# Kernel tuning notes

Measured on AMD Instinct MI355X. Metric: run time of the kernel, lower is better.

Reference implementation:

```python
import jax, jax.numpy as jnp
import numpy as np

EPS = 1e-6

def setup_inputs() -> dict:
    key = jax.random.key(0)
    ks = jax.random.split(key, 8)
    B, C, H, W = 8, 256, 128, 128
    d = C // 8  # scale=8
    return {
        "x": jax.random.normal(ks[0], (B, C, H, W), dtype=jnp.float32),
        "wq": jax.random.normal(ks[1], (d, C), dtype=jnp.float32) * 0.05,
        "bq": jax.random.normal(ks[2], (d,), dtype=jnp.float32) * 0.05,
        "wk": jax.random.normal(ks[3], (d, C), dtype=jnp.float32) * 0.05,
        "bk": jax.random.normal(ks[4], (d,), dtype=jnp.float32) * 0.05,
        "wv": jax.random.normal(ks[5], (C, C), dtype=jnp.float32) * 0.05,
        "bv": jax.random.normal(ks[6], (C,), dtype=jnp.float32) * 0.05,
        "gamma": jax.random.normal(ks[7], (1,), dtype=jnp.float32) * 0.05,
    }

def reference(x, wq, bq, wk, bk, wv, bv, gamma):
    B, C, H, W = x.shape
    N = H * W
    xf = x.reshape(B, C, N)  # flatten spatial
    # 1x1 convs == channel-mixing matmuls
    Q = jax.nn.softplus(jnp.einsum('dc,bcn->bnd', wq, xf) + bq[None, None, :])  # [B,N,d]
    K = jax.nn.softplus(jnp.einsum('dc,bcn->bdn', wk, xf) + bk[None, :, None])  # [B,d,N]
    V = jnp.einsum('ec,bcn->ben', wv, xf) + bv[None, :, None]                    # [B,C,N]
    KV = jnp.einsum('bmn,bcn->bmc', K, V)                # [B,d,C]
    norm = 1.0 / jnp.einsum('bnm,bm->bn', Q, K.sum(-1) + EPS)  # [B,N]
    wv_out = jnp.einsum('bnm,bmc,bn->bcn', Q, KV, norm)  # [B,C,N]
    return x + gamma * wv_out.reshape(B, C, H, W)
```

## Files before the change

### kernel.cpp

```cpp
#include <hip/hip_runtime.h>

#define NB 8
#define NC 256
#define ND 32
#define NN 16384
#define EPSF 1e-6f

__device__ __forceinline__ float softplusf(float v) {
    return fmaxf(v, 0.0f) + log1pf(__expf(-fabsf(v)));
}

__global__ __launch_bounds__(256) void kA(
    const float* __restrict__ x, const float* __restrict__ wk,
    const float* __restrict__ bk, float* __restrict__ part,
    float* __restrict__ kxf, float* __restrict__ ksum, int use_part)
{
    __shared__ __align__(16) float xsT[32 * 258];
    __shared__ __align__(16) float wkM[32 * 260];
    __shared__ __align__(16) float Ks [32 * 36];

    const int t    = threadIdx.x;
    const int b    = blockIdx.x >> 6;
    const int tile = blockIdx.x & 63;
    const int n0   = tile << 8;
    const float* xb = x + (size_t)b * NC * NN;

    #pragma unroll
    for (int i = 0; i < 32; ++i) {
        int f = t + (i << 8);
        wkM[(f >> 8) * 260 + (f & 255)] = wk[f];
    }

    const int jA  = t & 31;
    const int m0A = (t >> 5) << 2;
    const int m0X = (t >> 6) << 3;
    const int eX  = t & 63;

    float bkr[4];
    #pragma unroll
    for (int r = 0; r < 4; ++r) bkr[r] = bk[m0A + r];

    float acc[8][4];
    #pragma unroll
    for (int a = 0; a < 8; ++a)
        #pragma unroll
        for (int kk = 0; kk < 4; ++kk) acc[a][kk] = 0.0f;
    float ksacc[4] = {0.f, 0.f, 0.f, 0.f};

    for (int st = 0; st < 8; ++st) {
        const int n1 = n0 + (st << 5);
        __syncthreads();
        #pragma unroll
        for (int i = 0; i < 32; ++i) {
            int f = t + (i << 8);
            int c = f >> 5, j = f & 31;
            xsT[j * 258 + c] = xb[c * NN + n1 + j];
        }
        __syncthreads();

        float kacc[4] = {0.f, 0.f, 0.f, 0.f};
        #pragma unroll 4
        for (int c = 0; c < 256; c += 4) {
            float2 xa = *(const float2*)&xsT[jA * 258 + c];
            float2 xc = *(const float2*)&xsT[jA * 258 + c + 2];
            #pragma unroll
            for (int r = 0; r < 4; ++r) {
                float4 w = *(const float4*)&wkM[(m0A + r) * 260 + c];
                kacc[r] = fmaf(xa.x, w.x, kacc[r]);
                kacc[r] = fmaf(xa.y, w.y, kacc[r]);
                kacc[r] = fmaf(xc.x, w.z, kacc[r]);
                kacc[r] = fmaf(xc.y, w.w, kacc[r]);
            }
        }
        #pragma unroll
        for (int r = 0; r < 4; ++r) {
            float kv_ = softplusf(kacc[r] + bkr[r]);
            Ks[jA * 36 + m0A + r] = kv_;
            ksacc[r] += kv_;
        }
        __syncthreads();

        #pragma unroll 2
        for (int j = 0; j < 32; ++j) {
            const float* kp = &Ks[j * 36 + m0X];
            float4 ka = *(const float4*)kp;
            float4 kb = *(const float4*)(kp + 4);
            const float km[8] = {ka.x, ka.y, ka.z, ka.w, kb.x, kb.y, kb.z, kb.w};
            float xv[4];
            #pragma unroll
            for (int kk = 0; kk < 4; ++kk) xv[kk] = xsT[j * 258 + eX + (kk << 6)];
            #pragma unroll
            for (int a = 0; a < 8; ++a)
                #pragma unroll
                for (int kk = 0; kk < 4; ++kk)
                    acc[a][kk] = fmaf(km[a], xv[kk], acc[a][kk]);
        }
    }

    #pragma unroll
    for (int r = 0; r < 4; ++r) {
        float v = ksacc[r];
        for (int o = 16; o; o >>= 1) v += __shfl_down(v, o, 32);
        if (jA == 0) atomicAdd(&ksum[b * 32 + m0A + r], v);
    }

    if (use_part) {
        float* dst = part + (size_t)blockIdx.x * 8192;
        #pragma unroll
        for (int a = 0; a < 8; ++a)
            #pragma unroll
            for (int kk = 0; kk < 4; ++kk)
                dst[(m0X + a) * 256 + eX + (kk << 6)] = acc[a][kk];
    } else {
        float* dst = kxf + (size_t)b * 8192;
        #pragma unroll
        for (int a = 0; a < 8; ++a)
            #pragma unroll
            for (int kk = 0; kk < 4; ++kk)
                atomicAdd(&dst[(m0X + a) * 256 + eX + (kk << 6)], acc[a][kk]);
    }
}

__global__ __launch_bounds__(256) void kR(const float* __restrict__ part,
                                          float* __restrict__ kxf)
{
    int idx = blockIdx.x * 256 + threadIdx.x;
    int b = idx >> 13, f = idx & 8191;
    float s = 0.f;
    #pragma unroll 8
    for (int tl = 0; tl < 64; ++tl)
        s += part[(size_t)(b * 64 + tl) * 8192 + f];
    kxf[idx] = s;
}

__global__ __launch_bounds__(256) void kB(
    const float* __restrict__ kxf, const float* __restrict__ ksum,
    const float* __restrict__ wv, const float* __restrict__ bv,
    float* __restrict__ kv)
{
    __shared__ float wvT[256 * 33];
    __shared__ float kxs[32 * 257];

    const int t  = threadIdx.x;
    const int b  = blockIdx.x >> 3;
    const int c0 = (blockIdx.x & 7) << 5;

    #pragma unroll
    for (int i = 0; i < 32; ++i) {
        int f = t + (i << 8);
        int r = f >> 8, e = f & 255;
        wvT[e * 33 + r]  = wv[(size_t)(c0 + r) * 256 + e];
        kxs[r * 257 + e] = kxf[b * 8192 + f];
    }
    __syncthreads();

    const int cl = t & 31, mq = t >> 5;
    float a0 = 0.f, a1 = 0.f, a2 = 0.f, a3 = 0.f;
    for (int e = 0; e < 256; ++e) {
        float wvv = wvT[e * 33 + cl];
        a0 = fmaf(kxs[(mq     ) * 257 + e], wvv, a0);
        a1 = fmaf(kxs[(mq +  8) * 257 + e], wvv, a1);
        a2 = fmaf(kxs[(mq + 16) * 257 + e], wvv, a2);
        a3 = fmaf(kxs[(mq + 24) * 257 + e], wvv, a3);
    }
    const int c = c0 + cl;
    const float bvc = bv[c];
    const float* ks = ksum + b * 32;
    float* kvb = kv + (size_t)b * 8192;
    kvb[(mq     ) * 256 + c] = a0 + bvc * ks[mq     ];
    kvb[(mq +  8) * 256 + c] = a1 + bvc * ks[mq +  8];
    kvb[(mq + 16) * 256 + c] = a2 + bvc * ks[mq + 16];
    kvb[(mq + 24) * 256 + c] = a3 + bvc * ks[mq + 24];
}

__global__ __launch_bounds__(512) void kC(
    const float* __restrict__ x, const float* __restrict__ wq,
    const float* __restrict__ bq, const float* __restrict__ kv,
    const float* __restrict__ ksum, const float* __restrict__ gamma,
    float* __restrict__ out)
{
    __shared__ __align__(16) float xs [256 * 64];
    __shared__ __align__(16) float wqM[32 * 260];
    __shared__ __align__(16) float Qs [32 * 68];
    __shared__ __align__(16) float KVs[32 * 256];
    __shared__ float ksE[32];

    const int t    = threadIdx.x;
    const int b    = blockIdx.x >> 6;
    const int tile = blockIdx.x & 63;
    const int n0   = tile << 8;
    const float* xb = x + (size_t)b * NC * NN;
    const float g = gamma[0];

    #pragma unroll
    for (int i = 0; i < 16; ++i) {
        int f = t + (i << 9);
        wqM[(f >> 8) * 260 + (f & 255)] = wq[f];
        KVs[f] = kv[(size_t)b * 8192 + f];
    }
    if (t < 32) ksE[t] = ksum[b * 32 + t] + EPSF;

    const int jsQ = t & 15;
    const int mQ  = t >> 4;
    const float bqm = bq[mQ];
    const int jO  = t & 63;
    const int c0O = (t >> 6) << 5;

    for (int st = 0; st < 4; ++st) {
        const int n1 = n0 + (st << 6);
        __syncthreads();
        #pragma unroll
        for (int i = 0; i < 32; ++i) {
            int f = t + (i << 9);
            int c = f >> 6, j = f & 63;
            xs[f] = xb[c * NN + n1 + j];
        }
        __syncthreads();

        float qa[4] = {0.f, 0.f, 0.f, 0.f};
        #pragma unroll 4
        for (int c = 0; c < 256; c += 4) {
            float4 w  = *(const float4*)&wqM[mQ * 260 + c];
            float4 x0 = *(const float4*)&xs[(c + 0) * 64 + (jsQ << 2)];
            float4 x1 = *(const float4*)&xs[(c + 1) * 64 + (jsQ << 2)];
            float4 x2 = *(const float4*)&xs[(c + 2) * 64 + (jsQ << 2)];
            float4 x3 = *(const float4*)&xs[(c + 3) * 64 + (jsQ << 2)];
            qa[0] = fmaf(w.x, x0.x, qa[0]); qa[0] = fmaf(w.y, x1.x, qa[0]);
            qa[0] = fmaf(w.z, x2.x, qa[0]); qa[0] = fmaf(w.w, x3.x, qa[0]);
            qa[1] = fmaf(w.x, x0.y, qa[1]); qa[1] = fmaf(w.y, x1.y, qa[1]);
            qa[1] = fmaf(w.z, x2.y, qa[1]); qa[1] = fmaf(w.w, x3.y, qa[1]);
            qa[2] = fmaf(w.x, x0.z, qa[2]); qa[2] = fmaf(w.y, x1.z, qa[2]);
            qa[2] = fmaf(w.z, x2.z, qa[2]); qa[2] = fmaf(w.w, x3.z, qa[2]);
            qa[3] = fmaf(w.x, x0.w, qa[3]); qa[3] = fmaf(w.y, x1.w, qa[3]);
            qa[3] = fmaf(w.z, x2.w, qa[3]); qa[3] = fmaf(w.w, x3.w, qa[3]);
        }
        #pragma unroll
        for (int r = 0; r < 4; ++r)
            Qs[mQ * 68 + (jsQ << 2) + r] = softplusf(qa[r] + bqm);
        __syncthreads();

        float q[32];
        #pragma unroll
        for (int m = 0; m < 32; ++m) q[m] = Qs[m * 68 + jO];
        float den = 0.f;
        #pragma unroll
        for (int m = 0; m < 32; ++m) den = fmaf(q[m], ksE[m], den);
        const float nrm = g / den;

        #pragma unroll
        for (int cc = 0; cc < 8; ++cc) {
            const int c = c0O + (cc << 2);
            float s0 = 0.f, s1 = 0.f, s2 = 0.f, s3 = 0.f;
            #pragma unroll
            for (int m = 0; m < 32; ++m) {
                float4 kvv = *(const float4*)&KVs[m * 256 + c];
                s0 = fmaf(q[m], kvv.x, s0);
                s1 = fmaf(q[m], kvv.y, s1);
                s2 = fmaf(q[m], kvv.z, s2);
                s3 = fmaf(q[m], kvv.w, s3);
            }
            size_t base = (size_t)b * NC * NN + (size_t)c * NN + n1 + jO;
            out[base         ] = xs[(c + 0) * 64 + jO] + nrm * s0;
            out[base +     NN] = xs[(c + 1) * 64 + jO] + nrm * s1;
            out[base + 2 * NN] = xs[(c + 2) * 64 + jO] + nrm * s2;
            out[base + 3 * NN] = xs[(c + 3) * 64 + jO] + nrm * s3;
        }
    }
}

extern "C" void kernel_launch(void* const* d_in, const int* in_sizes, int n_in,
                              void* d_out, int out_size, void* d_ws, size_t ws_size,
                              hipStream_t stream)
{
    (void)in_sizes; (void)n_in; (void)out_size;
    const float* x     = (const float*)d_in[0];
    const float* wq    = (const float*)d_in[1];
    const float* bq    = (const float*)d_in[2];
    const float* wk    = (const float*)d_in[3];
    const float* bk    = (const float*)d_in[4];
    const float* wv    = (const float*)d_in[5];
    const float* bv    = (const float*)d_in[6];
    const float* gamma = (const float*)d_in[7];
    float* out = (float*)d_out;

    char* ws = (char*)d_ws;
    float* kxf  = (float*)(ws);
    float* ksum = (float*)(ws + 262144);
    float* kv   = (float*)(ws + 263168);
    float* part = (float*)(ws + 525312);
    const size_t need_part = 525312ull + 512ull * 8192ull * 4ull;
    const int use_part = (ws_size >= need_part) ? 1 : 0;

    hipMemsetAsync(ksum, 0, 1024, stream);
    if (!use_part) hipMemsetAsync(kxf, 0, 262144, stream);

    kA<<<dim3(512), dim3(256), 0, stream>>>(x, wk, bk, part, kxf, ksum, use_part);
    if (use_part) kR<<<dim3(256), dim3(256), 0, stream>>>(part, kxf);
    kB<<<dim3(64), dim3(256), 0, stream>>>(kxf, ksum, wv, bv, kv);
    kC<<<dim3(512), dim3(512), 0, stream>>>(x, wq, bq, kv, ksum, gamma, out);
}
```

Before: 431.4 us.

## Restructure output kernel with transposed weights, uniform scalar loads and smaller tiles

Adds a small kernel that transposes wq and makes kB write KV transposed as [C,d]. kC now runs 2048 blocks of 256 threads, each handling one 64-column tile instead of looping over four stages. Q is computed with per-wave channel splits reduced through shared-memory atomics, and weights and KV are read from global memory with wave-uniform addresses rather than staged in LDS. The aim is lower LDS use, higher occupancy and cheaper weight access, at the cost of shared-memory atomics, an extra launch and reliance on cached global reads.

Result: slower. 627.0 us (+45.3%).

```diff
diff --git a/kernel.cpp b/kernel.cpp
--- a/kernel.cpp
+++ b/kernel.cpp
@@ -8,6 +8,14 @@
 
 __device__ __forceinline__ float softplusf(float v) {
     return fmaxf(v, 0.0f) + log1pf(__expf(-fabsf(v)));
+}
+
+__global__ __launch_bounds__(256) void kT(const float* __restrict__ wq,
+                                          float* __restrict__ wqT)
+{
+    int idx = blockIdx.x * 256 + threadIdx.x;
+    int c = idx >> 5, m = idx & 31;
+    wqT[idx] = wq[m * 256 + c];
 }
 
 __global__ __launch_bounds__(256) void kA(
@@ -136,7 +144,7 @@
 __global__ __launch_bounds__(256) void kB(
     const float* __restrict__ kxf, const float* __restrict__ ksum,
     const float* __restrict__ wv, const float* __restrict__ bv,
-    float* __restrict__ kv)
+    float* __restrict__ kvT)
 {
     __shared__ float wvT[256 * 33];
     __shared__ float kxs[32 * 257];
@@ -166,104 +174,99 @@
     const int c = c0 + cl;
     const float bvc = bv[c];
     const float* ks = ksum + b * 32;
-    float* kvb = kv + (size_t)b * 8192;
-    kvb[(mq     ) * 256 + c] = a0 + bvc * ks[mq     ];
-    kvb[(mq +  8) * 256 + c] = a1 + bvc * ks[mq +  8];
-    kvb[(mq + 16) * 256 + c] = a2 + bvc * ks[mq + 16];
-    kvb[(mq + 24) * 256 + c] = a3 + bvc * ks[mq + 24];
-}
-
-__global__ __launch_bounds__(512) void kC(
-    const float* __restrict__ x, const float* __restrict__ wq,
-    const float* __restrict__ bq, const float* __restrict__ kv,
+    float* kvb = kvT + (size_t)b * 8192;
+    kvb[c * 32 + (mq     )] = a0 + bvc * ks[mq     ];
+    kvb[c * 32 + (mq +  8)] = a1 + bvc * ks[mq +  8];
+    kvb[c * 32 + (mq + 16)] = a2 + bvc * ks[mq + 16];
+    kvb[c * 32 + (mq + 24)] = a3 + bvc * ks[mq + 24];
+}
+
+__global__ __launch_bounds__(256) void kC(
+    const float* __restrict__ x, const float* __restrict__ wqT,
+    const float* __restrict__ bq, const float* __restrict__ kvT,
     const float* __restrict__ ksum, const float* __restrict__ gamma,
     float* __restrict__ out)
 {
-    __shared__ __align__(16) float xs [256 * 64];
-    __shared__ __align__(16) float wqM[32 * 260];
-    __shared__ __align__(16) float Qs [32 * 68];
-    __shared__ __align__(16) float KVs[32 * 256];
-    __shared__ float ksE[32];
+    __shared__ __align__(16) float xs[256 * 64];
+    __shared__ float Qs[64 * 33];
 
     const int t    = threadIdx.x;
-    const int b    = blockIdx.x >> 6;
-    const int tile = blockIdx.x & 63;
-    const int n0   = tile << 8;
-    const float* xb = x + (size_t)b * NC * NN;
-    const float g = gamma[0];
+    const int b    = blockIdx.x >> 8;
+    const int tile = blockIdx.x & 255;
+    const int n1   = tile << 6;
+    const float* __restrict__ xb  = x   + (size_t)b * NC * NN;
+    const float* __restrict__ kvb = kvT + (size_t)b * 8192;
+
+    #pragma unroll
+    for (int i = 0; i < 9; ++i) {
+        int f = t + (i << 8);
+        if (f < 64 * 33) Qs[f] = 0.0f;
+    }
 
     #pragma unroll
     for (int i = 0; i < 16; ++i) {
-        int f = t + (i << 9);
-        wqM[(f >> 8) * 260 + (f & 255)] = wq[f];
-        KVs[f] = kv[(size_t)b * 8192 + f];
-    }
-    if (t < 32) ksE[t] = ksum[b * 32 + t] + EPSF;
-
-    const int jsQ = t & 15;
-    const int mQ  = t >> 4;
-    const float bqm = bq[mQ];
-    const int jO  = t & 63;
-    const int c0O = (t >> 6) << 5;
-
-    for (int st = 0; st < 4; ++st) {
-        const int n1 = n0 + (st << 6);
-        __syncthreads();
-        #pragma unroll
-        for (int i = 0; i < 32; ++i) {
-            int f = t + (i << 9);
-            int c = f >> 6, j = f & 63;
-            xs[f] = xb[c * NN + n1 + j];
-        }
-        __syncthreads();
-
-        float qa[4] = {0.f, 0.f, 0.f, 0.f};
-        #pragma unroll 4
-        for (int c = 0; c < 256; c += 4) {
-            float4 w  = *(const float4*)&wqM[mQ * 260 + c];
-            float4 x0 = *(const float4*)&xs[(c + 0) * 64 + (jsQ << 2)];
-            float4 x1 = *(const float4*)&xs[(c + 1) * 64 + (jsQ << 2)];
-            float4 x2 = *(const float4*)&xs[(c + 2) * 64 + (jsQ << 2)];
-            float4 x3 = *(const float4*)&xs[(c + 3) * 64 + (jsQ << 2)];
-            qa[0] = fmaf(w.x, x0.x, qa[0]); qa[0] = fmaf(w.y, x1.x, qa[0]);
-            qa[0] = fmaf(w.z, x2.x, qa[0]); qa[0] = fmaf(w.w, x3.x, qa[0]);
-            qa[1] = fmaf(w.x, x0.y, qa[1]); qa[1] = fmaf(w.y, x1.y, qa[1]);
-            qa[1] = fmaf(w.z, x2.y, qa[1]); qa[1] = fmaf(w.w, x3.y, qa[1]);
-            qa[2] = fmaf(w.x, x0.z, qa[2]); qa[2] = fmaf(w.y, x1.z, qa[2]);
-            qa[2] = fmaf(w.z, x2.z, qa[2]); qa[2] = fmaf(w.w, x3.z, qa[2]);
-            qa[3] = fmaf(w.x, x0.w, qa[3]); qa[3] = fmaf(w.y, x1.w, qa[3]);
-            qa[3] = fmaf(w.z, x2.w, qa[3]); qa[3] = fmaf(w.w, x3.w, qa[3]);
-        }
-        #pragma unroll
-        for (int r = 0; r < 4; ++r)
-            Qs[mQ * 68 + (jsQ << 2) + r] = softplusf(qa[r] + bqm);
-        __syncthreads();
-
+        int q4 = t + (i << 8);
+        int c = q4 >> 4, jq = q4 & 15;
+        *(float4*)&xs[c * 64 + (jq << 2)] =
+            *(const float4*)&xb[(size_t)c * NN + n1 + (jq << 2)];
+    }
+    __syncthreads();
+
+    const int lane = t & 63;
+    const int w    = t >> 6;
+
+    {
+        float qp[32];
+        #pragma unroll
+        for (int m = 0; m < 32; ++m) qp[m] = 0.0f;
+        const int cbase = w << 6;
+        #pragma unroll 2
+        for (int i = 0; i < 64; ++i) {
+            const int c = cbase + i;
+            const float xv = xs[c * 64 + lane];
+            const float* __restrict__ wr = wqT + c * 32;
+            #pragma unroll
+            for (int m = 0; m < 32; ++m)
+                qp[m] = fmaf(wr[m], xv, qp[m]);
+        }
+        #pragma unroll
+        for (int m = 0; m < 32; ++m)
+            atomicAdd(&Qs[lane * 33 + m], qp[m]);
+    }
+    __syncthreads();
+
+    {
+        const int col = t & 63, ms = t >> 6;
+        #pragma unroll
+        for (int r = 0; r < 8; ++r) {
+            const int m = (ms << 3) + r;
+            Qs[col * 33 + m] = softplusf(Qs[col * 33 + m] + bq[m]);
+        }
+    }
+    __syncthreads();
+
+    {
+        const int j = lane, cg = w;
         float q[32];
         #pragma unroll
-        for (int m = 0; m < 32; ++m) q[m] = Qs[m * 68 + jO];
-        float den = 0.f;
-        #pragma unroll
-        for (int m = 0; m < 32; ++m) den = fmaf(q[m], ksE[m], den);
-        const float nrm = g / den;
-
-        #pragma unroll
-        for (int cc = 0; cc < 8; ++cc) {
-            const int c = c0O + (cc << 2);
-            float s0 = 0.f, s1 = 0.f, s2 = 0.f, s3 = 0.f;
-            #pragma unroll
-            for (int m = 0; m < 32; ++m) {
-                float4 kvv = *(const float4*)&KVs[m * 256 + c];
-                s0 = fmaf(q[m], kvv.x, s0);
-                s1 = fmaf(q[m], kvv.y, s1);
-                s2 = fmaf(q[m], kvv.z, s2);
-                s3 = fmaf(q[m], kvv.w, s3);
-            }
-            size_t base = (size_t)b * NC * NN + (size_t)c * NN + n1 + jO;
-            out[base         ] = xs[(c + 0) * 64 + jO] + nrm * s0;
-            out[base +     NN] = xs[(c + 1) * 64 + jO] + nrm * s1;
-            out[base + 2 * NN] = xs[(c + 2) * 64 + jO] + nrm * s2;
-            out[base + 3 * NN] = xs[(c + 3) * 64 + jO] + nrm * s3;
+        for (int m = 0; m < 32; ++m) q[m] = Qs[j * 33 + m];
+        const float* __restrict__ ksb = ksum + (b << 5);
+        float den = 0.0f;
+        #pragma unroll
+        for (int m = 0; m < 32; ++m) den = fmaf(q[m], ksb[m] + EPSF, den);
+        const float nrm = gamma[0] / den;
+
+        const int cbase = cg << 6;
+        float* __restrict__ ob = out + (size_t)b * NC * NN + n1 + j;
+        #pragma unroll 2
+        for (int i = 0; i < 64; ++i) {
+            const int c = cbase + i;
+            const float* __restrict__ kr = kvb + c * 32;
+            float s = 0.0f;
+            #pragma unroll
+            for (int m = 0; m < 32; ++m)
+                s = fmaf(kr[m], q[m], s);
+            ob[(size_t)c * NN] = xs[c * 64 + j] + nrm * s;
         }
     }
 }
@@ -286,16 +289,18 @@
     char* ws = (char*)d_ws;
     float* kxf  = (float*)(ws);
     float* ksum = (float*)(ws + 262144);
-    float* kv   = (float*)(ws + 263168);
-    float* part = (float*)(ws + 525312);
-    const size_t need_part = 525312ull + 512ull * 8192ull * 4ull;
+    float* kvT  = (float*)(ws + 263168);
+    float* wqT  = (float*)(ws + 525312);
+    float* part = (float*)(ws + 558080);
+    const size_t need_part = 558080ull + 512ull * 8192ull * 4ull;
     const int use_part = (ws_size >= need_part) ? 1 : 0;
 
     hipMemsetAsync(ksum, 0, 1024, stream);
     if (!use_part) hipMemsetAsync(kxf, 0, 262144, stream);
 
+    kT<<<dim3(32), dim3(256), 0, stream>>>(wq, wqT);
     kA<<<dim3(512), dim3(256), 0, stream>>>(x, wk, bk, part, kxf, ksum, use_part);
     if (use_part) kR<<<dim3(256), dim3(256), 0, stream>>>(part, kxf);
-    kB<<<dim3(64), dim3(256), 0, stream>>>(kxf, ksum, wv, bv, kv);
-    kC<<<dim3(512), dim3(512), 0, stream>>>(x, wq, bq, kv, ksum, gamma, out);
-}
+    kB<<<dim3(64), dim3(256), 0, stream>>>(kxf, ksum, wv, bv, kvT);
+    kC<<<dim3(2048), dim3(256), 0, stream>>>(x, wqT, bq, kvT, ksum, gamma, out);
+}
```

## Split final stage into Q-normalization kernel and register-tiled output kernel

Applied to the files above, without the earlier changes.

The fused output kernel kC is replaced by two kernels when the workspace is large enough. kQ computes softplus(Q), divides by the denominator, scales by gamma and writes qhat to the workspace. kO then applies a 4x16 register-blocked Q·KV product per thread over smaller tiles with more blocks, and adds the residual. This aims for better occupancy and compute efficiency in the output stage, at the cost of an extra 16 MB write and read of qhat, one more kernel launch, and a second read of x.

After: 439.7 us. Within noise of the previous version (+1.9%).

```diff
diff --git a/kernel.cpp b/kernel.cpp
--- a/kernel.cpp
+++ b/kernel.cpp
@@ -171,6 +171,146 @@
     kvb[(mq +  8) * 256 + c] = a1 + bvc * ks[mq +  8];
     kvb[(mq + 16) * 256 + c] = a2 + bvc * ks[mq + 16];
     kvb[(mq + 24) * 256 + c] = a3 + bvc * ks[mq + 24];
+}
+
+__global__ __launch_bounds__(256) void kQ(
+    const float* __restrict__ x, const float* __restrict__ wq,
+    const float* __restrict__ bq, const float* __restrict__ ksum,
+    const float* __restrict__ gamma, float* __restrict__ qhat)
+{
+    __shared__ __align__(16) float xsT[32 * 258];
+    __shared__ __align__(16) float wqM[32 * 260];
+    __shared__ float den_s[32];
+
+    const int t    = threadIdx.x;
+    const int b    = blockIdx.x >> 6;
+    const int tile = blockIdx.x & 63;
+    const int n0   = tile << 8;
+    const float* xb = x + (size_t)b * NC * NN;
+    const float g = gamma[0];
+
+    #pragma unroll
+    for (int i = 0; i < 32; ++i) {
+        int f = t + (i << 8);
+        wqM[(f >> 8) * 260 + (f & 255)] = wq[f];
+    }
+
+    const int jA  = t & 31;
+    const int m0A = (t >> 5) << 2;
+
+    float bqr[4], ksr[4];
+    #pragma unroll
+    for (int r = 0; r < 4; ++r) {
+        bqr[r] = bq[m0A + r];
+        ksr[r] = ksum[b * 32 + m0A + r] + EPSF;
+    }
+
+    for (int st = 0; st < 8; ++st) {
+        const int n1 = n0 + (st << 5);
+        __syncthreads();
+        #pragma unroll
+        for (int i = 0; i < 32; ++i) {
+            int f = t + (i << 8);
+            int c = f >> 5, j = f & 31;
+            xsT[j * 258 + c] = xb[c * NN + n1 + j];
+        }
+        if (t < 32) den_s[t] = 0.0f;
+        __syncthreads();
+
+        float kacc[4] = {0.f, 0.f, 0.f, 0.f};
+        #pragma unroll 4
+        for (int c = 0; c < 256; c += 4) {
+            float2 xa = *(const float2*)&xsT[jA * 258 + c];
+            float2 xc = *(const float2*)&xsT[jA * 258 + c + 2];
+            #pragma unroll
+            for (int r = 0; r < 4; ++r) {
+                float4 w = *(const float4*)&wqM[(m0A + r) * 260 + c];
+                kacc[r] = fmaf(xa.x, w.x, kacc[r]);
+                kacc[r] = fmaf(xa.y, w.y, kacc[r]);
+                kacc[r] = fmaf(xc.x, w.z, kacc[r]);
+                kacc[r] = fmaf(xc.y, w.w, kacc[r]);
+            }
+        }
+        float qv[4];
+        float pd = 0.0f;
+        #pragma unroll
+        for (int r = 0; r < 4; ++r) {
+            qv[r] = softplusf(kacc[r] + bqr[r]);
+            pd = fmaf(qv[r], ksr[r], pd);
+        }
+        atomicAdd(&den_s[jA], pd);
+        __syncthreads();
+
+        const float nrm = g / den_s[jA];
+        #pragma unroll
+        for (int r = 0; r < 4; ++r)
+            qhat[(size_t)(b * 32 + m0A + r) * NN + n1 + jA] = qv[r] * nrm;
+    }
+}
+
+__global__ __launch_bounds__(256) void kO(
+    const float* __restrict__ x, const float* __restrict__ qhat,
+    const float* __restrict__ kv, float* __restrict__ out)
+{
+    __shared__ __align__(16) float KVs[32 * 256];
+    __shared__ __align__(16) float Qs [32 * 68];
+
+    const int t    = threadIdx.x;
+    const int b    = blockIdx.x >> 8;
+    const int tile = blockIdx.x & 255;
+    const int n1   = tile << 6;
+
+    #pragma unroll
+    for (int i = 0; i < 32; ++i)
+        KVs[t + (i << 8)] = kv[b * 8192 + t + (i << 8)];
+    #pragma unroll
+    for (int i = 0; i < 8; ++i) {
+        int f = t + (i << 8);
+        int m = f >> 6, j = f & 63;
+        Qs[m * 68 + j] = qhat[(size_t)(b * 32 + m) * NN + n1 + j];
+    }
+    __syncthreads();
+
+    const int jq = t & 15;
+    const int cg = t >> 4;
+
+    float acc[4][16];
+    #pragma unroll
+    for (int a = 0; a < 4; ++a)
+        #pragma unroll
+        for (int ci = 0; ci < 16; ++ci) acc[a][ci] = 0.0f;
+
+    #pragma unroll 8
+    for (int m = 0; m < 32; ++m) {
+        float4 q  = *(const float4*)&Qs[m * 68 + (jq << 2)];
+        const float* kr = &KVs[m * 256 + (cg << 4)];
+        float4 k0 = *(const float4*)(kr     );
+        float4 k1 = *(const float4*)(kr +  4);
+        float4 k2 = *(const float4*)(kr +  8);
+        float4 k3 = *(const float4*)(kr + 12);
+        const float kk[16] = {k0.x, k0.y, k0.z, k0.w, k1.x, k1.y, k1.z, k1.w,
+                              k2.x, k2.y, k2.z, k2.w, k3.x, k3.y, k3.z, k3.w};
+        const float qq[4] = {q.x, q.y, q.z, q.w};
+        #pragma unroll
+        for (int ci = 0; ci < 16; ++ci)
+            #pragma unroll
+            for (int a = 0; a < 4; ++a)
+                acc[a][ci] = fmaf(qq[a], kk[ci], acc[a][ci]);
+    }
+
+    const float* __restrict__ xb = x   + (size_t)b * NC * NN + n1 + (jq << 2);
+    float* __restrict__       ob = out + (size_t)b * NC * NN + n1 + (jq << 2);
+    #pragma unroll
+    for (int ci = 0; ci < 16; ++ci) {
+        const int c = (cg << 4) + ci;
+        float4 xv = *(const float4*)&xb[(size_t)c * NN];
+        float4 ov;
+        ov.x = xv.x + acc[0][ci];
+        ov.y = xv.y + acc[1][ci];
+        ov.z = xv.z + acc[2][ci];
+        ov.w = xv.w + acc[3][ci];
+        *(float4*)&ob[(size_t)c * NN] = ov;
+    }
 }
 
 __global__ __launch_bounds__(512) void kC(
@@ -287,15 +427,21 @@
     float* kxf  = (float*)(ws);
     float* ksum = (float*)(ws + 262144);
     float* kv   = (float*)(ws + 263168);
-    float* part = (float*)(ws + 525312);
-    const size_t need_part = 525312ull + 512ull * 8192ull * 4ull;
-    const int use_part = (ws_size >= need_part) ? 1 : 0;
+    float* big  = (float*)(ws + 525312);
+    const size_t need_big = 525312ull + 16777216ull;
+    const int use_big = (ws_size >= need_big) ? 1 : 0;
 
     hipMemsetAsync(ksum, 0, 1024, stream);
-    if (!use_part) hipMemsetAsync(kxf, 0, 262144, stream);
-
-    kA<<<dim3(512), dim3(256), 0, stream>>>(x, wk, bk, part, kxf, ksum, use_part);
-    if (use_part) kR<<<dim3(256), dim3(256), 0, stream>>>(part, kxf);
+    if (!use_big) hipMemsetAsync(kxf, 0, 262144, stream);
+
+    kA<<<dim3(512), dim3(256), 0, stream>>>(x, wk, bk, big, kxf, ksum, use_big);
+    if (use_big) kR<<<dim3(256), dim3(256), 0, stream>>>(big, kxf);
     kB<<<dim3(64), dim3(256), 0, stream>>>(kxf, ksum, wv, bv, kv);
-    kC<<<dim3(512), dim3(512), 0, stream>>>(x, wq, bq, kv, ksum, gamma, out);
-}
+    if (use_big) {
+        float* qhat = big;
+        kQ<<<dim3(512), dim3(256), 0, stream>>>(x, wq, bq, ksum, gamma, qhat);
+        kO<<<dim3(2048), dim3(256), 0, stream>>>(x, qhat, kv, out);
+    } else {
+        kC<<<dim3(512), dim3(512), 0, stream>>>(x, wq, bq, kv, ksum, gamma, out);
+    }
+}
```
